# Performance work log

Measured on AMD Instinct MI355X. Metric: run time of the kernel, lower is better.

The kernel has to match this reference:

```python
import jax, jax.numpy as jnp
import numpy as np

D = 1024      # n_embd
H = 2048      # expert_hidden_dim
G = 4         # num_groups
EPG = 2       # experts_per_group
NH = 16       # num_heads
HD = D // NH  # head dim
L = 4         # num_layers
V = 32000     # vocab_size
NC = 32000    # num_classes
MAXS = 2048   # max_seq_len
B, S = 2, 1024
TEMP = 1.0    # router_temperature


def setup_inputs() -> dict:
    key = jax.random.key(0)
    ks = jax.random.split(key, 12)
    sc = 0.02
    def n(k, shape):
        return jax.random.normal(k, shape, jnp.float32) * sc
    return {
        "x": jax.random.randint(ks[0], (B, S), 0, V),
        "tok_emb": n(ks[1], (V, D)),
        "pos_emb": n(ks[2], (MAXS, D)),
        "in_proj_w": n(ks[3], (L, 3 * D, D)),
        "in_proj_b": jnp.zeros((L, 3 * D)),
        "out_w": n(ks[4], (L, D, D)),
        "out_b": jnp.zeros((L, D)),
        "ln1_w": jnp.ones((L, D)), "ln1_b": jnp.zeros((L, D)),
        "ln2_w": jnp.ones((L, D)), "ln2_b": jnp.zeros((L, D)),
        "gr_w": n(ks[5], (L, D, G)), "gr_b": jnp.zeros((L, G)),
        "er_w": n(ks[6], (L, G, D, EPG)), "er_b": jnp.zeros((L, G, EPG)),
        "w1": n(ks[7], (L, G, EPG, D, H)), "b1": jnp.zeros((L, G, EPG, H)),
        "w2": n(ks[8], (L, G, EPG, H, D)), "b2": jnp.zeros((L, G, EPG, D)),
        "lnf_w": jnp.ones((D,)), "lnf_b": jnp.zeros((D,)),
        "head_w": n(ks[9], (NC, D)), "head_b": jnp.zeros((NC,)),
    }


def _ln(x, w, b):
    m = x.mean(-1, keepdims=True)
    v = ((x - m) ** 2).mean(-1, keepdims=True)
    return (x - m) * jax.lax.rsqrt(v + 1e-5) * w + b


def _attn(x, wqkv, bqkv, wo, bo, mask):
    b, s, _ = x.shape
    qkv = x @ wqkv.T + bqkv
    q, k, v = jnp.split(qkv, 3, axis=-1)
    def heads(t):
        return t.reshape(b, s, NH, HD).transpose(0, 2, 1, 3)
    q, k, v = heads(q), heads(k), heads(v)
    sc = jnp.einsum('bhqd,bhkd->bhqk', q, k) / np.float32(np.sqrt(HD))
    sc = jnp.where(mask, sc, jnp.float32(-1e30))
    a = jax.nn.softmax(sc, axis=-1)
    o = jnp.einsum('bhqk,bhkd->bhqd', a, v).transpose(0, 2, 1, 3).reshape(b, s, D)
    return o @ wo.T + bo


def _moe(x, gw, gb, ew, eb, w1, b1, w2, b2):
    # x: [T, D] flattened tokens. 2-level routing: top-1 group, top-1 expert in group.
    gp = jax.nn.softmax((x @ gw + gb) / TEMP, axis=-1)                      # [T,G]
    gidx = jnp.argmax(gp, axis=-1)                                          # [T]
    ep = jax.nn.softmax((jnp.einsum('td,gde->tge', x, ew) + eb) / TEMP, -1)  # [T,G,EPG]
    ep_sel = jnp.take_along_axis(ep, gidx[:, None, None], axis=1)[:, 0]     # [T,EPG]
    eidx = jnp.argmax(ep_sel, axis=-1)                                      # [T]
    gate = (jnp.take_along_axis(gp, gidx[:, None], 1)[:, 0]
            * jnp.take_along_axis(ep_sel, eidx[:, None], 1)[:, 0])          # [T]
    hmid = jax.nn.relu(jnp.einsum('td,gedh->tgeh', x, w1) + b1)             # [T,G,EPG,H]
    out = jnp.einsum('tgeh,gehd->tged', hmid, w2) + b2                      # [T,G,EPG,D]
    comb = (jax.nn.one_hot(gidx, G, dtype=x.dtype)[:, :, None]
            * jax.nn.one_hot(eidx, EPG, dtype=x.dtype)[:, None, :]) * gate[:, None, None]
    return jnp.einsum('tge,tged->td', comb, out)


def reference(x, tok_emb, pos_emb, in_proj_w, in_proj_b, out_w, out_b,
              ln1_w, ln1_b, ln2_w, ln2_b, gr_w, gr_b, er_w, er_b,
              w1, b1, w2, b2, lnf_w, lnf_b, head_w, head_b):
    b, s = x.shape
    h = tok_emb[x] + pos_emb[jnp.arange(s)][None]
    mask = jnp.tril(jnp.ones((s, s), bool))
    for l in range(L):
        x1 = _ln(h, ln1_w[l], ln1_b[l])
        h = h + _attn(x1, in_proj_w[l], in_proj_b[l], out_w[l], out_b[l], mask)
        x2 = _ln(h, ln2_w[l], ln2_b[l]).reshape(b * s, D)
        h = h + _moe(x2, gr_w[l], gr_b[l], er_w[l], er_b[l],
                     w1[l], b1[l], w2[l], b2[l]).reshape(b, s, D)
    h = _ln(h, lnf_w, lnf_b).mean(axis=1)
    return h @ head_w.T + head_b
```

## Files before the change

kernel.cpp:

```cpp
#include <hip/hip_runtime.h>
#include <hip/hip_bf16.h>
#include <cstdint>
#include <cstddef>

#define D_   1024
#define H_   2048
#define G_   4
#define EPG_ 2
#define NE_  8
#define NH_  16
#define HD_  64
#define L_   4
#define V_   32000
#define NC_  32000
#define B_   2
#define S_   1024
#define T_   2048

typedef __attribute__((__ext_vector_type__(8))) __bf16 bf16x8;
typedef __attribute__((__ext_vector_type__(4))) __bf16 bf16x4;
typedef __attribute__((__ext_vector_type__(4))) float  f32x4;

__device__ __forceinline__ void gl_lds16(const void* g, void* l) {
  __builtin_amdgcn_global_load_lds(
      (const __attribute__((address_space(1))) void*)g,
      (__attribute__((address_space(3))) void*)l, 16, 0, 0);
}

__global__ __launch_bounds__(256) void embed_kernel(const int* __restrict__ x,
    const float* __restrict__ tok, const float* __restrict__ pos,
    float* __restrict__ h) {
  int t = blockIdx.x;
  int tid = threadIdx.x;
  int token = x[t];
  int s = t & (S_ - 1);
  float4 tv = *(const float4*)(tok + (size_t)token * D_ + tid * 4);
  float4 pv = *(const float4*)(pos + (size_t)s * D_ + tid * 4);
  float4 r;
  r.x = tv.x + pv.x; r.y = tv.y + pv.y; r.z = tv.z + pv.z; r.w = tv.w + pv.w;
  *(float4*)(h + (size_t)t * D_ + tid * 4) = r;
}

__device__ __forceinline__ float block_sum256(float v, float* sbuf) {
  #pragma unroll
  for (int o = 32; o >= 1; o >>= 1) v += __shfl_xor(v, o, 64);
  int tid = threadIdx.x;
  if ((tid & 63) == 0) sbuf[tid >> 6] = v;
  __syncthreads();
  float r = sbuf[0] + sbuf[1] + sbuf[2] + sbuf[3];
  __syncthreads();
  return r;
}

template<bool F32OUT, bool BFOUT>
__global__ __launch_bounds__(256) void ln_kernel(const float* __restrict__ X,
    const float* __restrict__ w, const float* __restrict__ b,
    float* __restrict__ Yf, __bf16* __restrict__ Yb) {
  __shared__ float sbuf[4];
  int t = blockIdx.x, tid = threadIdx.x;
  const float* xr = X + (size_t)t * D_;
  float4 v = *(const float4*)(xr + tid * 4);
  float sum = v.x + v.y + v.z + v.w;
  float m = block_sum256(sum, sbuf) * (1.0f / D_);
  float dx = v.x - m, dy = v.y - m, dz = v.z - m, dw = v.w - m;
  float vs = dx * dx + dy * dy + dz * dz + dw * dw;
  float var = block_sum256(vs, sbuf) * (1.0f / D_);
  float rs = rsqrtf(var + 1e-5f);
  float4 wv = *(const float4*)(w + tid * 4);
  float4 bv = *(const float4*)(b + tid * 4);
  float4 o;
  o.x = dx * rs * wv.x + bv.x;
  o.y = dy * rs * wv.y + bv.y;
  o.z = dz * rs * wv.z + bv.z;
  o.w = dw * rs * wv.w + bv.w;
  if (F32OUT) *(float4*)(Yf + (size_t)t * D_ + tid * 4) = o;
  if (BFOUT) {
    bf16x4 ob = {(__bf16)o.x, (__bf16)o.y, (__bf16)o.z, (__bf16)o.w};
    *(bf16x4*)(Yb + (size_t)t * D_ + tid * 4) = ob;
  }
}

template<int MODE, int NF, bool KN>
__global__ __launch_bounds__(256) void gemm_mfma(
    const __bf16* __restrict__ A, const float* __restrict__ W,
    const float* __restrict__ bias, float* __restrict__ Cf,
    __bf16* __restrict__ Cb, const int* __restrict__ tlist,
    const int* __restrict__ offs, const int* __restrict__ counts,
    const float* __restrict__ gate, int N, int K) {
  __shared__ __bf16 As[128 * 64];
  __shared__ __bf16 Bs[NF * 32 * 64];
  int e = blockIdx.z;
  int cnt = (MODE >= 2) ? counts[e] : T_;
  int row0 = blockIdx.y * 128;
  if (row0 >= cnt) return;
  int lbase = (MODE >= 2) ? offs[e] : 0;
  int col0 = blockIdx.x * (NF * 32);
  const float* Wp = W + (size_t)e * N * K;
  const float* bp = bias + (size_t)e * N;
  int tid = threadIdx.x;
  int w = tid >> 6, lane = tid & 63, lq = lane & 15, lg = lane >> 4;
  int wr = w >> 1, wc = w & 1;

  const __bf16* asrc[4];
  #pragma unroll
  for (int it = 0; it < 4; it++) {
    int v = it * 256 + tid;
    int r = v >> 3, u = v & 7;
    int gr = row0 + r;
    long rowidx;
    if (MODE >= 2) rowidx = tlist[lbase + ((gr < cnt) ? gr : cnt - 1)];
    else rowidx = gr;
    asrc[it] = A + (size_t)rowidx * K + (u ^ (r & 7)) * 8;
  }
  const float* bsrc[NF];
  int bdst[NF];
  #pragma unroll
  for (int it = 0; it < NF; it++) {
    if (!KN) {
      int v = it * 256 + tid;
      int n = v >> 3, u = v & 7;
      bsrc[it] = Wp + (size_t)(col0 + n) * K + u * 8;
      bdst[it] = n * 64 + (u ^ (n & 7)) * 8;
    } else {
      int v = it * 256 + tid;
      int n = v & (NF * 32 - 1), u = v / (NF * 32);
      bsrc[it] = Wp + (size_t)(u * 8) * N + col0 + n;
      bdst[it] = n * 64 + (u ^ (n & 7)) * 8;
    }
  }

  f32x4 acc[4][NF] = {};
  for (int k0 = 0; k0 < K; k0 += 64) {
    #pragma unroll
    for (int it = 0; it < 4; it++)
      gl_lds16(asrc[it] + k0, &As[(it * 256 + tid) * 8]);
    #pragma unroll
    for (int it = 0; it < NF; it++) {
      float f[8];
      if (!KN) {
        float4 f0 = *(const float4*)(bsrc[it] + k0);
        float4 f1 = *(const float4*)(bsrc[it] + k0 + 4);
        f[0] = f0.x; f[1] = f0.y; f[2] = f0.z; f[3] = f0.w;
        f[4] = f1.x; f[5] = f1.y; f[6] = f1.z; f[7] = f1.w;
      } else {
        #pragma unroll
        for (int j = 0; j < 8; j++)
          f[j] = bsrc[it][(size_t)(k0 + j) * N];
      }
      bf16x8 bb = {(__bf16)f[0], (__bf16)f[1], (__bf16)f[2], (__bf16)f[3],
                   (__bf16)f[4], (__bf16)f[5], (__bf16)f[6], (__bf16)f[7]};
      *(bf16x8*)&Bs[bdst[it]] = bb;
    }
    __syncthreads();
    #pragma unroll
    for (int kk = 0; kk < 2; kk++) {
      bf16x8 a[4], b[NF];
      int us = ((lg + kk * 4) ^ (lq & 7)) * 8;
      #pragma unroll
      for (int fi = 0; fi < 4; fi++)
        a[fi] = *(const bf16x8*)&As[(wr * 64 + fi * 16 + lq) * 64 + us];
      #pragma unroll
      for (int fj = 0; fj < NF; fj++)
        b[fj] = *(const bf16x8*)&Bs[(wc * (NF * 16) + fj * 16 + lq) * 64 + us];
      #pragma unroll
      for (int fi = 0; fi < 4; fi++)
        #pragma unroll
        for (int fj = 0; fj < NF; fj++)
          acc[fi][fj] = __builtin_amdgcn_mfma_f32_16x16x32_bf16(a[fi], b[fj], acc[fi][fj], 0, 0, 0);
    }
    __syncthreads();
  }

  #pragma unroll
  for (int fi = 0; fi < 4; fi++) {
    #pragma unroll
    for (int v = 0; v < 4; v++) {
      int r = row0 + wr * 64 + fi * 16 + lg * 4 + v;
      long orow;
      float gv = 1.f;
      if (MODE >= 2) {
        if (r >= cnt) continue;
        orow = tlist[lbase + r];
        if (MODE == 3) gv = gate[orow];
      } else {
        orow = r;
      }
      #pragma unroll
      for (int fj = 0; fj < NF; fj++) {
        int c = col0 + wc * (NF * 16) + fj * 16 + lq;
        float val = acc[fi][fj][v] + bp[c];
        if (MODE == 0)      Cb[orow * N + c] = (__bf16)val;
        else if (MODE == 1) Cf[orow * N + c] += val;
        else if (MODE == 2) Cb[orow * N + c] = (__bf16)fmaxf(val, 0.f);
        else                Cf[orow * N + c] += gv * val;
      }
    }
  }
}

#define SC_LOG2 0.18033688011112042f
__global__ __launch_bounds__(256) void attn_mfma_kernel(const __bf16* __restrict__ qkv,
                                                        __bf16* __restrict__ out) {
  __shared__ __bf16 Ks[64][72];
  __shared__ __bf16 Vt[64][72];
  __shared__ __bf16 Ps[64][72];
  int tid = threadIdx.x;
  int w = tid >> 6, lane = tid & 63, lq = lane & 15, lg = lane >> 4;
  int qt = blockIdx.x, b = blockIdx.y >> 4, hh = blockIdx.y & 15;
  const __bf16* qbase = qkv + (size_t)b * S_ * 3 * D_ + hh * HD_;

  bf16x8 qa[2];
  {
    const __bf16* qp = qbase + (size_t)(qt * 64 + w * 16 + lq) * 3 * D_ + lg * 8;
    qa[0] = *(const bf16x8*)qp;
    qa[1] = *(const bf16x8*)(qp + 32);
  }

  f32x4 o[4] = {};
  float m_[4] = {-1e30f, -1e30f, -1e30f, -1e30f};
  float l_[4] = {0.f, 0.f, 0.f, 0.f};

  for (int kt = 0; kt <= qt; kt++) {
    #pragma unroll
    for (int it = 0; it < 2; it++) {
      int idx = tid + it * 256;
      int row = idx >> 3, c8 = idx & 7;
      const __bf16* kp = qbase + (size_t)(kt * 64 + row) * 3 * D_ + D_ + c8 * 8;
      *(bf16x8*)&Ks[row][c8 * 8] = *(const bf16x8*)kp;
      bf16x8 vv = *(const bf16x8*)(kp + D_);
      #pragma unroll
      for (int j = 0; j < 8; j++) Vt[c8 * 8 + j][row] = vv[j];
    }
    __syncthreads();

    f32x4 s[4] = {};
    #pragma unroll
    for (int kk = 0; kk < 2; kk++)
      #pragma unroll
      for (int fc = 0; fc < 4; fc++) {
        bf16x8 kf = *(const bf16x8*)&Ks[fc * 16 + lq][lg * 8 + kk * 32];
        s[fc] = __builtin_amdgcn_mfma_f32_16x16x32_bf16(qa[kk], kf, s[fc], 0, 0, 0);
      }

    #pragma unroll
    for (int fc = 0; fc < 4; fc++)
      #pragma unroll
      for (int v = 0; v < 4; v++) {
        float sv = s[fc][v] * SC_LOG2;
        if (kt == qt && (fc * 16 + lq) > (w * 16 + lg * 4 + v)) sv = -1e30f;
        s[fc][v] = sv;
      }

    float corr[4];
    #pragma unroll
    for (int v = 0; v < 4; v++) {
      float rm = fmaxf(fmaxf(s[0][v], s[1][v]), fmaxf(s[2][v], s[3][v]));
      #pragma unroll
      for (int o2 = 8; o2 >= 1; o2 >>= 1) rm = fmaxf(rm, __shfl_xor(rm, o2, 64));
      float mnew = fmaxf(m_[v], rm);
      float cc = exp2f(m_[v] - mnew);
      float rs = 0.f;
      #pragma unroll
      for (int fc = 0; fc < 4; fc++) {
        float p = exp2f(s[fc][v] - mnew);
        s[fc][v] = p; rs += p;
      }
      l_[v] = l_[v] * cc + rs;
      m_[v] = mnew;
      corr[v] = cc;
    }
    #pragma unroll
    for (int dc = 0; dc < 4; dc++)
      #pragma unroll
      for (int v = 0; v < 4; v++) o[dc][v] *= corr[v];

    #pragma unroll
    for (int fc = 0; fc < 4; fc++)
      #pragma unroll
      for (int v = 0; v < 4; v++)
        Ps[w * 16 + lg * 4 + v][fc * 16 + lq] = (__bf16)s[fc][v];
    __syncthreads();

    #pragma unroll
    for (int kk = 0; kk < 2; kk++) {
      bf16x8 pa = *(const bf16x8*)&Ps[w * 16 + lq][lg * 8 + kk * 32];
      #pragma unroll
      for (int dc = 0; dc < 4; dc++) {
        bf16x8 vb = *(const bf16x8*)&Vt[dc * 16 + lq][lg * 8 + kk * 32];
        o[dc] = __builtin_amdgcn_mfma_f32_16x16x32_bf16(pa, vb, o[dc], 0, 0, 0);
      }
    }
    __syncthreads();
  }

  #pragma unroll
  for (int v = 0; v < 4; v++) {
    float ls = l_[v];
    #pragma unroll
    for (int o2 = 8; o2 >= 1; o2 >>= 1) ls += __shfl_xor(ls, o2, 64);
    float inv = 1.0f / ls;
    int row = qt * 64 + w * 16 + lg * 4 + v;
    __bf16* op = out + ((size_t)b * S_ + row) * D_ + hh * HD_;
    #pragma unroll
    for (int dc = 0; dc < 4; dc++)
      op[dc * 16 + lq] = (__bf16)(o[dc][v] * inv);
  }
}

__global__ __launch_bounds__(64) void route_kernel(const float* __restrict__ X,
    const float* __restrict__ gw, const float* __restrict__ gb,
    const float* __restrict__ ew, const float* __restrict__ eb,
    int* __restrict__ eidx, float* __restrict__ gate) {
  int t = blockIdx.x;
  int lane = threadIdx.x;
  const float* xr = X + (size_t)t * D_;
  float g0 = 0, g1 = 0, g2 = 0, g3 = 0;
  #pragma unroll
  for (int k = 0; k < 16; k++) {
    int d = lane + 64 * k;
    float xv = xr[d];
    float4 gv = *(const float4*)(gw + (size_t)d * G_);
    g0 += xv * gv.x; g1 += xv * gv.y; g2 += xv * gv.z; g3 += xv * gv.w;
  }
  #pragma unroll
  for (int o = 32; o >= 1; o >>= 1) {
    g0 += __shfl_xor(g0, o, 64); g1 += __shfl_xor(g1, o, 64);
    g2 += __shfl_xor(g2, o, 64); g3 += __shfl_xor(g3, o, 64);
  }
  g0 += gb[0]; g1 += gb[1]; g2 += gb[2]; g3 += gb[3];
  float mx = fmaxf(fmaxf(g0, g1), fmaxf(g2, g3));
  float p0 = __expf(g0 - mx), p1 = __expf(g1 - mx), p2 = __expf(g2 - mx), p3 = __expf(g3 - mx);
  float psum = p0 + p1 + p2 + p3;
  int gidx = 0; float best = g0;
  if (g1 > best) { best = g1; gidx = 1; }
  if (g2 > best) { best = g2; gidx = 2; }
  if (g3 > best) { best = g3; gidx = 3; }
  float gpsel = ((gidx == 0) ? p0 : (gidx == 1) ? p1 : (gidx == 2) ? p2 : p3) / psum;

  const float* ewg = ew + (size_t)gidx * D_ * EPG_;
  float e0 = 0, e1 = 0;
  #pragma unroll
  for (int k = 0; k < 16; k++) {
    int d = lane + 64 * k;
    float xv = xr[d];
    float2 ev = *(const float2*)(ewg + (size_t)d * EPG_);
    e0 += xv * ev.x; e1 += xv * ev.y;
  }
  #pragma unroll
  for (int o = 32; o >= 1; o >>= 1) {
    e0 += __shfl_xor(e0, o, 64); e1 += __shfl_xor(e1, o, 64);
  }
  e0 += eb[gidx * EPG_ + 0]; e1 += eb[gidx * EPG_ + 1];
  float em = fmaxf(e0, e1);
  float q0 = __expf(e0 - em), q1 = __expf(e1 - em);
  int ei = (e1 > e0) ? 1 : 0;
  float epsel = ((ei == 0) ? q0 : q1) / (q0 + q1);
  if (lane == 0) {
    eidx[t] = gidx * EPG_ + ei;
    gate[t] = gpsel * epsel;
  }
}

__global__ __launch_bounds__(256) void finalize_kernel(const int* __restrict__ eidx,
    int* __restrict__ counts, int* __restrict__ offs, int* __restrict__ tlist) {
  __shared__ int hist[256][NE_];
  __shared__ int eoff[NE_];
  int tid = threadIdx.x;
  int loc[NE_];
  #pragma unroll
  for (int e = 0; e < NE_; e++) loc[e] = 0;
  int te[8];
  #pragma unroll
  for (int i = 0; i < 8; i++) { te[i] = eidx[tid * 8 + i]; loc[te[i]]++; }
  #pragma unroll
  for (int e = 0; e < NE_; e++) hist[tid][e] = loc[e];
  __syncthreads();
  for (int off = 1; off < 256; off <<= 1) {
    int v[NE_];
    #pragma unroll
    for (int e = 0; e < NE_; e++) v[e] = (tid >= off) ? hist[tid - off][e] : 0;
    __syncthreads();
    #pragma unroll
    for (int e = 0; e < NE_; e++) hist[tid][e] += v[e];
    __syncthreads();
  }
  if (tid == 0) {
    int acc = 0;
    for (int e = 0; e < NE_; e++) {
      int c = hist[255][e];
      eoff[e] = acc; counts[e] = c; offs[e] = acc; acc += c;
    }
  }
  __syncthreads();
  int run[NE_];
  #pragma unroll
  for (int e = 0; e < NE_; e++) run[e] = eoff[e] + hist[tid][e] - loc[e];
  #pragma unroll
  for (int i = 0; i < 8; i++) {
    int e = te[i];
    tlist[run[e]++] = tid * 8 + i;
  }
}

__global__ __launch_bounds__(256) void mean_part_kernel(const float* __restrict__ X,
                                                        float* __restrict__ part) {
  int bd = blockIdx.x * 256 + threadIdx.x;
  int chunk = blockIdx.y;
  int b = bd >> 10, d = bd & 1023;
  float s = 0.f;
  #pragma unroll 4
  for (int i = 0; i < 64; i++) {
    int sidx = chunk * 64 + i;
    s += X[((size_t)b * S_ + sidx) * D_ + d];
  }
  part[chunk * T_ + bd] = s;
}

__global__ __launch_bounds__(256) void mean_final_kernel(const float* __restrict__ part,
                                                         float* __restrict__ hm) {
  int bd = blockIdx.x * 256 + threadIdx.x;
  float s = 0.f;
  #pragma unroll
  for (int c = 0; c < 16; c++) s += part[c * T_ + bd];
  hm[bd] = s * (1.0f / S_);
}

__global__ __launch_bounds__(256) void head_kernel(const float* __restrict__ hm,
    const float* __restrict__ hw, const float* __restrict__ hb,
    float* __restrict__ out) {
  int w = threadIdx.x >> 6;
  int lane = threadIdx.x & 63;
  int c = blockIdx.x * 4 + w;
  const float* row = hw + (size_t)c * D_;
  float acc0 = 0.f, acc1 = 0.f;
  #pragma unroll
  for (int k = 0; k < 4; k++) {
    int d = lane * 4 + k * 256;
    float4 wv = *(const float4*)(row + d);
    float4 h0 = *(const float4*)(hm + d);
    float4 h1 = *(const float4*)(hm + D_ + d);
    acc0 += wv.x * h0.x + wv.y * h0.y + wv.z * h0.z + wv.w * h0.w;
    acc1 += wv.x * h1.x + wv.y * h1.y + wv.z * h1.z + wv.w * h1.w;
  }
  #pragma unroll
  for (int o = 32; o >= 1; o >>= 1) {
    acc0 += __shfl_xor(acc0, o, 64);
    acc1 += __shfl_xor(acc1, o, 64);
  }
  if (lane == 0) {
    float bias = hb[c];
    out[c] = acc0 + bias;
    out[NC_ + c] = acc1 + bias;
  }
}

extern "C" void kernel_launch(void* const* d_in, const int* in_sizes, int n_in,
                              void* d_out, int out_size, void* d_ws, size_t ws_size,
                              hipStream_t stream) {
  const int*   x        = (const int*)d_in[0];
  const float* tok_emb  = (const float*)d_in[1];
  const float* pos_emb  = (const float*)d_in[2];
  const float* in_proj_w= (const float*)d_in[3];
  const float* in_proj_b= (const float*)d_in[4];
  const float* out_w    = (const float*)d_in[5];
  const float* out_b    = (const float*)d_in[6];
  const float* ln1_w    = (const float*)d_in[7];
  const float* ln1_b    = (const float*)d_in[8];
  const float* ln2_w    = (const float*)d_in[9];
  const float* ln2_b    = (const float*)d_in[10];
  const float* gr_w     = (const float*)d_in[11];
  const float* gr_b     = (const float*)d_in[12];
  const float* er_w     = (const float*)d_in[13];
  const float* er_b     = (const float*)d_in[14];
  const float* w1       = (const float*)d_in[15];
  const float* b1       = (const float*)d_in[16];
  const float* w2       = (const float*)d_in[17];
  const float* b2       = (const float*)d_in[18];
  const float* lnf_w    = (const float*)d_in[19];
  const float* lnf_b    = (const float*)d_in[20];
  const float* head_w   = (const float*)d_in[21];
  const float* head_b   = (const float*)d_in[22];

  char* wp = (char*)d_ws;
  auto carve = [&](size_t bytes) -> char* {
    char* p = wp;
    wp += (bytes + 255) & ~(size_t)255;
    return p;
  };
  float*  h      = (float*)carve((size_t)T_ * D_ * 4);
  float*  x1     = (float*)carve((size_t)T_ * D_ * 4);
  __bf16* x1b    = (__bf16*)carve((size_t)T_ * D_ * 2);
  __bf16* qkvb   = (__bf16*)carve((size_t)T_ * 3 * D_ * 2);
  __bf16* attnb  = (__bf16*)carve((size_t)T_ * D_ * 2);
  __bf16* hmidb  = (__bf16*)carve((size_t)T_ * H_ * 2);
  float*  part   = (float*)carve((size_t)16 * T_ * 4);
  float*  hm     = (float*)carve((size_t)B_ * D_ * 4);
  float*  gate   = (float*)carve((size_t)T_ * 4);
  int*    eidx   = (int*)carve((size_t)T_ * 4);
  int*    tlist  = (int*)carve((size_t)T_ * 4);
  int*    counts = (int*)carve(64);
  int*    offs   = (int*)carve(64);

  embed_kernel<<<T_, 256, 0, stream>>>(x, tok_emb, pos_emb, h);

  for (int l = 0; l < L_; l++) {
    ln_kernel<false, true><<<T_, 256, 0, stream>>>(h, ln1_w + l * D_, ln1_b + l * D_,
                                                   nullptr, x1b);
    gemm_mfma<0, 4, false><<<dim3(24, 16, 1), 256, 0, stream>>>(
        x1b, in_proj_w + (size_t)l * 3 * D_ * D_, in_proj_b + (size_t)l * 3 * D_,
        nullptr, qkvb, nullptr, nullptr, nullptr, nullptr, 3 * D_, D_);
    attn_mfma_kernel<<<dim3(S_ / 64, B_ * NH_), 256, 0, stream>>>(qkvb, attnb);
    gemm_mfma<1, 2, false><<<dim3(16, 16, 1), 256, 0, stream>>>(
        attnb, out_w + (size_t)l * D_ * D_, out_b + (size_t)l * D_, h, nullptr,
        nullptr, nullptr, nullptr, nullptr, D_, D_);

    ln_kernel<true, true><<<T_, 256, 0, stream>>>(h, ln2_w + l * D_, ln2_b + l * D_,
                                                  x1, x1b);
    route_kernel<<<T_, 64, 0, stream>>>(x1,
        gr_w + (size_t)l * D_ * G_, gr_b + (size_t)l * G_,
        er_w + (size_t)l * G_ * D_ * EPG_, er_b + (size_t)l * G_ * EPG_,
        eidx, gate);
    finalize_kernel<<<1, 256, 0, stream>>>(eidx, counts, offs, tlist);

    gemm_mfma<2, 4, true><<<dim3(H_ / 128, T_ / 128, NE_), 256, 0, stream>>>(
        x1b, w1 + (size_t)l * NE_ * D_ * H_, b1 + (size_t)l * NE_ * H_, nullptr, hmidb,
        tlist, offs, counts, nullptr, H_, D_);
    gemm_mfma<3, 2, true><<<dim3(D_ / 64, T_ / 128, NE_), 256, 0, stream>>>(
        hmidb, w2 + (size_t)l * NE_ * H_ * D_, b2 + (size_t)l * NE_ * D_, h, nullptr,
        tlist, offs, counts, gate, D_, H_);
  }

  ln_kernel<true, false><<<T_, 256, 0, stream>>>(h, lnf_w, lnf_b, x1, nullptr);
  mean_part_kernel<<<dim3(B_ * D_ / 256, 16), 256, 0, stream>>>(x1, part);
  mean_final_kernel<<<B_ * D_ / 256, 256, 0, stream>>>(part, hm);
  head_kernel<<<NC_ / 4, 256, 0, stream>>>(hm, head_w, head_b, (float*)d_out);
}
```

Measured before the change: 1.037 ms.

## Fuse LN2 with routing, compact MoE tile grid, prefetch GEMM weights, reverse attention order

LayerNorm2 and the two-level router are merged into one kernel that keeps the normalized row in registers, removing the fp32 x1 round trip and one launch. The finalize step now emits a compact list of (expert, row-tile) blocks, so the expert GEMMs launch at most 24 row tiles instead of an 8x16 grid that mostly exits early. The GEMM main loop double-buffers the fp32 weight loads in registers so the next tile's global reads overlap the current MFMA phase, and launch bounds request two blocks per CU. Attention blocks are issued in reverse query-tile order so the longest causal tiles start first. The register prefetch raises register pressure and could limit occupancy.

```diff
diff --git a/kernel.cpp b/kernel.cpp
--- a/kernel.cpp
+++ b/kernel.cpp
@@ -16,6 +16,7 @@
 #define B_   2
 #define S_   1024
 #define T_   2048
+#define MAXBLK_ 24
 
 typedef __attribute__((__ext_vector_type__(8))) __bf16 bf16x8;
 typedef __attribute__((__ext_vector_type__(4))) __bf16 bf16x4;
@@ -25,6 +26,12 @@
   __builtin_amdgcn_global_load_lds(
       (const __attribute__((address_space(1))) void*)g,
       (__attribute__((address_space(3))) void*)l, 16, 0, 0);
+}
+
+__device__ __forceinline__ float wave_sum(float v) {
+  #pragma unroll
+  for (int o = 32; o >= 1; o >>= 1) v += __shfl_xor(v, o, 64);
+  return v;
 }
 
 __global__ __launch_bounds__(256) void embed_kernel(const int* __restrict__ x,
@@ -42,8 +49,7 @@
 }
 
 __device__ __forceinline__ float block_sum256(float v, float* sbuf) {
-  #pragma unroll
-  for (int o = 32; o >= 1; o >>= 1) v += __shfl_xor(v, o, 64);
+  v = wave_sum(v);
   int tid = threadIdx.x;
   if ((tid & 63) == 0) sbuf[tid >> 6] = v;
   __syncthreads();
@@ -80,19 +86,147 @@
   }
 }
 
+__global__ __launch_bounds__(256) void ln_route_kernel(const float* __restrict__ X,
+    const float* __restrict__ lw, const float* __restrict__ lb,
+    const float* __restrict__ gw, const float* __restrict__ gb,
+    const float* __restrict__ ew, const float* __restrict__ eb,
+    __bf16* __restrict__ Yb, int* __restrict__ eidx, float* __restrict__ gate) {
+  int wv = threadIdx.x >> 6, lane = threadIdx.x & 63;
+  int t = blockIdx.x * 4 + wv;
+  const float* xr = X + (size_t)t * D_;
+  float4 xv[4];
+  #pragma unroll
+  for (int k = 0; k < 4; k++) xv[k] = *(const float4*)(xr + lane * 4 + k * 256);
+  float s = 0.f;
+  #pragma unroll
+  for (int k = 0; k < 4; k++) s += xv[k].x + xv[k].y + xv[k].z + xv[k].w;
+  float m = wave_sum(s) * (1.0f / D_);
+  float vs = 0.f;
+  #pragma unroll
+  for (int k = 0; k < 4; k++) {
+    float a = xv[k].x - m, b2 = xv[k].y - m, c = xv[k].z - m, d = xv[k].w - m;
+    vs += a * a + b2 * b2 + c * c + d * d;
+  }
+  float rs = rsqrtf(wave_sum(vs) * (1.0f / D_) + 1e-5f);
+  float y[4][4];
+  #pragma unroll
+  for (int k = 0; k < 4; k++) {
+    int d0 = lane * 4 + k * 256;
+    float4 wv4 = *(const float4*)(lw + d0);
+    float4 bv4 = *(const float4*)(lb + d0);
+    y[k][0] = (xv[k].x - m) * rs * wv4.x + bv4.x;
+    y[k][1] = (xv[k].y - m) * rs * wv4.y + bv4.y;
+    y[k][2] = (xv[k].z - m) * rs * wv4.z + bv4.z;
+    y[k][3] = (xv[k].w - m) * rs * wv4.w + bv4.w;
+    bf16x4 ob = {(__bf16)y[k][0], (__bf16)y[k][1], (__bf16)y[k][2], (__bf16)y[k][3]};
+    *(bf16x4*)(Yb + (size_t)t * D_ + d0) = ob;
+  }
+  float g0 = 0, g1 = 0, g2 = 0, g3 = 0;
+  #pragma unroll
+  for (int k = 0; k < 4; k++)
+    #pragma unroll
+    for (int j = 0; j < 4; j++) {
+      int d = lane * 4 + k * 256 + j;
+      float4 gv = *(const float4*)(gw + (size_t)d * G_);
+      float yv = y[k][j];
+      g0 += yv * gv.x; g1 += yv * gv.y; g2 += yv * gv.z; g3 += yv * gv.w;
+    }
+  g0 = wave_sum(g0) + gb[0];
+  g1 = wave_sum(g1) + gb[1];
+  g2 = wave_sum(g2) + gb[2];
+  g3 = wave_sum(g3) + gb[3];
+  float mx = fmaxf(fmaxf(g0, g1), fmaxf(g2, g3));
+  float p0 = __expf(g0 - mx), p1 = __expf(g1 - mx), p2 = __expf(g2 - mx), p3 = __expf(g3 - mx);
+  float psum = p0 + p1 + p2 + p3;
+  int gidx = 0; float best = g0;
+  if (g1 > best) { best = g1; gidx = 1; }
+  if (g2 > best) { best = g2; gidx = 2; }
+  if (g3 > best) { best = g3; gidx = 3; }
+  float gpsel = ((gidx == 0) ? p0 : (gidx == 1) ? p1 : (gidx == 2) ? p2 : p3) / psum;
+  const float* ewg = ew + (size_t)gidx * D_ * EPG_;
+  float e0 = 0, e1 = 0;
+  #pragma unroll
+  for (int k = 0; k < 4; k++)
+    #pragma unroll
+    for (int j = 0; j < 4; j++) {
+      int d = lane * 4 + k * 256 + j;
+      float2 ev = *(const float2*)(ewg + (size_t)d * EPG_);
+      e0 += y[k][j] * ev.x; e1 += y[k][j] * ev.y;
+    }
+  e0 = wave_sum(e0) + eb[gidx * EPG_ + 0];
+  e1 = wave_sum(e1) + eb[gidx * EPG_ + 1];
+  float em = fmaxf(e0, e1);
+  float q0 = __expf(e0 - em), q1 = __expf(e1 - em);
+  int ei = (e1 > e0) ? 1 : 0;
+  float epsel = ((ei == 0) ? q0 : q1) / (q0 + q1);
+  if (lane == 0) {
+    eidx[t] = gidx * EPG_ + ei;
+    gate[t] = gpsel * epsel;
+  }
+}
+
+__global__ __launch_bounds__(256) void finalize_kernel(const int* __restrict__ eidx,
+    int* __restrict__ counts, int* __restrict__ offs, int* __restrict__ tlist,
+    int* __restrict__ blk) {
+  __shared__ int hist[256][NE_];
+  __shared__ int eoff[NE_];
+  int tid = threadIdx.x;
+  int loc[NE_];
+  #pragma unroll
+  for (int e = 0; e < NE_; e++) loc[e] = 0;
+  int te[8];
+  #pragma unroll
+  for (int i = 0; i < 8; i++) { te[i] = eidx[tid * 8 + i]; loc[te[i]]++; }
+  #pragma unroll
+  for (int e = 0; e < NE_; e++) hist[tid][e] = loc[e];
+  __syncthreads();
+  for (int off = 1; off < 256; off <<= 1) {
+    int v[NE_];
+    #pragma unroll
+    for (int e = 0; e < NE_; e++) v[e] = (tid >= off) ? hist[tid - off][e] : 0;
+    __syncthreads();
+    #pragma unroll
+    for (int e = 0; e < NE_; e++) hist[tid][e] += v[e];
+    __syncthreads();
+  }
+  if (tid == 0) {
+    int acc = 0, nb = 0;
+    for (int e = 0; e < NE_; e++) {
+      int c = hist[255][e];
+      eoff[e] = acc; counts[e] = c; offs[e] = acc; acc += c;
+      for (int mt = 0; mt * 128 < c; mt++) blk[nb++] = e | (mt << 8);
+    }
+    for (; nb < MAXBLK_; nb++) blk[nb] = -1;
+  }
+  __syncthreads();
+  int run[NE_];
+  #pragma unroll
+  for (int e = 0; e < NE_; e++) run[e] = eoff[e] + hist[tid][e] - loc[e];
+  #pragma unroll
+  for (int i = 0; i < 8; i++) {
+    int e = te[i];
+    tlist[run[e]++] = tid * 8 + i;
+  }
+}
+
 template<int MODE, int NF, bool KN>
-__global__ __launch_bounds__(256) void gemm_mfma(
+__global__ __launch_bounds__(256, 2) void gemm_mfma(
     const __bf16* __restrict__ A, const float* __restrict__ W,
     const float* __restrict__ bias, float* __restrict__ Cf,
     __bf16* __restrict__ Cb, const int* __restrict__ tlist,
     const int* __restrict__ offs, const int* __restrict__ counts,
-    const float* __restrict__ gate, int N, int K) {
+    const float* __restrict__ gate, const int* __restrict__ blk,
+    int N, int K) {
   __shared__ __bf16 As[128 * 64];
   __shared__ __bf16 Bs[NF * 32 * 64];
-  int e = blockIdx.z;
-  int cnt = (MODE >= 2) ? counts[e] : T_;
-  int row0 = blockIdx.y * 128;
-  if (row0 >= cnt) return;
+  int e = 0, mt = blockIdx.y, cnt = T_;
+  if (MODE >= 2) {
+    int bv = blk[blockIdx.y];
+    if (bv < 0) return;
+    e = bv & 255; mt = bv >> 8;
+    cnt = counts[e];
+  }
+  int row0 = mt * 128;
   int lbase = (MODE >= 2) ? offs[e] : 0;
   int col0 = blockIdx.x * (NF * 32);
   const float* Wp = W + (size_t)e * N * K;
@@ -129,29 +263,42 @@
     }
   }
 
+  float br0[NF * 8], br1[NF * 8];
   f32x4 acc[4][NF] = {};
-  for (int k0 = 0; k0 < K; k0 += 64) {
-    #pragma unroll
-    for (int it = 0; it < 4; it++)
-      gl_lds16(asrc[it] + k0, &As[(it * 256 + tid) * 8]);
+
+  auto loadB = [&](float* br, int k0) {
     #pragma unroll
     for (int it = 0; it < NF; it++) {
-      float f[8];
       if (!KN) {
         float4 f0 = *(const float4*)(bsrc[it] + k0);
         float4 f1 = *(const float4*)(bsrc[it] + k0 + 4);
-        f[0] = f0.x; f[1] = f0.y; f[2] = f0.z; f[3] = f0.w;
-        f[4] = f1.x; f[5] = f1.y; f[6] = f1.z; f[7] = f1.w;
+        br[it * 8 + 0] = f0.x; br[it * 8 + 1] = f0.y;
+        br[it * 8 + 2] = f0.z; br[it * 8 + 3] = f0.w;
+        br[it * 8 + 4] = f1.x; br[it * 8 + 5] = f1.y;
+        br[it * 8 + 6] = f1.z; br[it * 8 + 7] = f1.w;
       } else {
         #pragma unroll
         for (int j = 0; j < 8; j++)
-          f[j] = bsrc[it][(size_t)(k0 + j) * N];
+          br[it * 8 + j] = bsrc[it][(size_t)(k0 + j) * N];
       }
-      bf16x8 bb = {(__bf16)f[0], (__bf16)f[1], (__bf16)f[2], (__bf16)f[3],
-                   (__bf16)f[4], (__bf16)f[5], (__bf16)f[6], (__bf16)f[7]};
+    }
+  };
+  auto writeB = [&](const float* br) {
+    #pragma unroll
+    for (int it = 0; it < NF; it++) {
+      bf16x8 bb = {(__bf16)br[it * 8 + 0], (__bf16)br[it * 8 + 1],
+                   (__bf16)br[it * 8 + 2], (__bf16)br[it * 8 + 3],
+                   (__bf16)br[it * 8 + 4], (__bf16)br[it * 8 + 5],
+                   (__bf16)br[it * 8 + 6], (__bf16)br[it * 8 + 7]};
       *(bf16x8*)&Bs[bdst[it]] = bb;
     }
-    __syncthreads();
+  };
+  auto stageA = [&](int k0) {
+    #pragma unroll
+    for (int it = 0; it < 4; it++)
+      gl_lds16(asrc[it] + k0, &As[(it * 256 + tid) * 8]);
+  };
+  auto mfmaPhase = [&]() {
     #pragma unroll
     for (int kk = 0; kk < 2; kk++) {
       bf16x8 a[4], b[NF];
@@ -168,6 +315,21 @@
         for (int fj = 0; fj < NF; fj++)
           acc[fi][fj] = __builtin_amdgcn_mfma_f32_16x16x32_bf16(a[fi], b[fj], acc[fi][fj], 0, 0, 0);
     }
+  };
+
+  loadB(br0, 0);
+  for (int k0 = 0; k0 < K; k0 += 128) {
+    stageA(k0);
+    writeB(br0);
+    loadB(br1, k0 + 64);
+    __syncthreads();
+    mfmaPhase();
+    __syncthreads();
+    stageA(k0 + 64);
+    writeB(br1);
+    if (k0 + 128 < K) loadB(br0, k0 + 128);
+    __syncthreads();
+    mfmaPhase();
     __syncthreads();
   }
 
@@ -206,7 +368,8 @@
   __shared__ __bf16 Ps[64][72];
   int tid = threadIdx.x;
   int w = tid >> 6, lane = tid & 63, lq = lane & 15, lg = lane >> 4;
-  int qt = blockIdx.x, b = blockIdx.y >> 4, hh = blockIdx.y & 15;
+  int qt = (S_ / 64 - 1) - blockIdx.x;
+  int b = blockIdx.y >> 4, hh = blockIdx.y & 15;
   const __bf16* qbase = qkv + (size_t)b * S_ * 3 * D_ + hh * HD_;
 
   bf16x8 qa[2];
@@ -304,101 +467,6 @@
     #pragma unroll
     for (int dc = 0; dc < 4; dc++)
       op[dc * 16 + lq] = (__bf16)(o[dc][v] * inv);
-  }
-}
-
-__global__ __launch_bounds__(64) void route_kernel(const float* __restrict__ X,
-    const float* __restrict__ gw, const float* __restrict__ gb,
-    const float* __restrict__ ew, const float* __restrict__ eb,
-    int* __restrict__ eidx, float* __restrict__ gate) {
-  int t = blockIdx.x;
-  int lane = threadIdx.x;
-  const float* xr = X + (size_t)t * D_;
-  float g0 = 0, g1 = 0, g2 = 0, g3 = 0;
-  #pragma unroll
-  for (int k = 0; k < 16; k++) {
-    int d = lane + 64 * k;
-    float xv = xr[d];
-    float4 gv = *(const float4*)(gw + (size_t)d * G_);
-    g0 += xv * gv.x; g1 += xv * gv.y; g2 += xv * gv.z; g3 += xv * gv.w;
-  }
-  #pragma unroll
-  for (int o = 32; o >= 1; o >>= 1) {
-    g0 += __shfl_xor(g0, o, 64); g1 += __shfl_xor(g1, o, 64);
-    g2 += __shfl_xor(g2, o, 64); g3 += __shfl_xor(g3, o, 64);
-  }
-  g0 += gb[0]; g1 += gb[1]; g2 += gb[2]; g3 += gb[3];
-  float mx = fmaxf(fmaxf(g0, g1), fmaxf(g2, g3));
-  float p0 = __expf(g0 - mx), p1 = __expf(g1 - mx), p2 = __expf(g2 - mx), p3 = __expf(g3 - mx);
-  float psum = p0 + p1 + p2 + p3;
-  int gidx = 0; float best = g0;
-  if (g1 > best) { best = g1; gidx = 1; }
-  if (g2 > best) { best = g2; gidx = 2; }
-  if (g3 > best) { best = g3; gidx = 3; }
-  float gpsel = ((gidx == 0) ? p0 : (gidx == 1) ? p1 : (gidx == 2) ? p2 : p3) / psum;
-
-  const float* ewg = ew + (size_t)gidx * D_ * EPG_;
-  float e0 = 0, e1 = 0;
-  #pragma unroll
-  for (int k = 0; k < 16; k++) {
-    int d = lane + 64 * k;
-    float xv = xr[d];
-    float2 ev = *(const float2*)(ewg + (size_t)d * EPG_);
-    e0 += xv * ev.x; e1 += xv * ev.y;
-  }
-  #pragma unroll
-  for (int o = 32; o >= 1; o >>= 1) {
-    e0 += __shfl_xor(e0, o, 64); e1 += __shfl_xor(e1, o, 64);
-  }
-  e0 += eb[gidx * EPG_ + 0]; e1 += eb[gidx * EPG_ + 1];
-  float em = fmaxf(e0, e1);
-  float q0 = __expf(e0 - em), q1 = __expf(e1 - em);
-  int ei = (e1 > e0) ? 1 : 0;
-  float epsel = ((ei == 0) ? q0 : q1) / (q0 + q1);
-  if (lane == 0) {
-    eidx[t] = gidx * EPG_ + ei;
-    gate[t] = gpsel * epsel;
-  }
-}
-
-__global__ __launch_bounds__(256) void finalize_kernel(const int* __restrict__ eidx,
-    int* __restrict__ counts, int* __restrict__ offs, int* __restrict__ tlist) {
-  __shared__ int hist[256][NE_];
-  __shared__ int eoff[NE_];
-  int tid = threadIdx.x;
-  int loc[NE_];
-  #pragma unroll
-  for (int e = 0; e < NE_; e++) loc[e] = 0;
-  int te[8];
-  #pragma unroll
-  for (int i = 0; i < 8; i++) { te[i] = eidx[tid * 8 + i]; loc[te[i]]++; }
-  #pragma unroll
-  for (int e = 0; e < NE_; e++) hist[tid][e] = loc[e];
-  __syncthreads();
-  for (int off = 1; off < 256; off <<= 1) {
-    int v[NE_];
-    #pragma unroll
-    for (int e = 0; e < NE_; e++) v[e] = (tid >= off) ? hist[tid - off][e] : 0;
-    __syncthreads();
-    #pragma unroll
-    for (int e = 0; e < NE_; e++) hist[tid][e] += v[e];
-    __syncthreads();
-  }
-  if (tid == 0) {
-    int acc = 0;
-    for (int e = 0; e < NE_; e++) {
-      int c = hist[255][e];
-      eoff[e] = acc; counts[e] = c; offs[e] = acc; acc += c;
-    }
-  }
-  __syncthreads();
-  int run[NE_];
-  #pragma unroll
-  for (int e = 0; e < NE_; e++) run[e] = eoff[e] + hist[tid][e] - loc[e];
-  #pragma unroll
-  for (int i = 0; i < 8; i++) {
-    int e = te[i];
-    tlist[run[e]++] = tid * 8 + i;
   }
 }
 
@@ -500,6 +568,7 @@
   int*    tlist  = (int*)carve((size_t)T_ * 4);
   int*    counts = (int*)carve(64);
   int*    offs   = (int*)carve(64);
+  int*    blk    = (int*)carve(MAXBLK_ * 4);
 
   embed_kernel<<<T_, 256, 0, stream>>>(x, tok_emb, pos_emb, h);
 
@@ -508,26 +577,25 @@
                                                    nullptr, x1b);
     gemm_mfma<0, 4, false><<<dim3(24, 16, 1), 256, 0, stream>>>(
         x1b, in_proj_w + (size_t)l * 3 * D_ * D_, in_proj_b + (size_t)l * 3 * D_,
-        nullptr, qkvb, nullptr, nullptr, nullptr, nullptr, 3 * D_, D_);
+        nullptr, qkvb, nullptr, nullptr, nullptr, nullptr, nullptr, 3 * D_, D_);
     attn_mfma_kernel<<<dim3(S_ / 64, B_ * NH_), 256, 0, stream>>>(qkvb, attnb);
     gemm_mfma<1, 2, false><<<dim3(16, 16, 1), 256, 0, stream>>>(
         attnb, out_w + (size_t)l * D_ * D_, out_b + (size_t)l * D_, h, nullptr,
-        nullptr, nullptr, nullptr, nullptr, D_, D_);
-
-    ln_kernel<true, true><<<T_, 256, 0, stream>>>(h, ln2_w + l * D_, ln2_b + l * D_,
-                                                  x1, x1b);
-    route_kernel<<<T_, 64, 0, stream>>>(x1,
+        nullptr, nullptr, nullptr, nullptr, nullptr, D_, D_);
+
+    ln_route_kernel<<<T_ / 4, 256, 0, stream>>>(h,
+        ln2_w + l * D_, ln2_b + l * D_,
         gr_w + (size_t)l * D_ * G_, gr_b + (size_t)l * G_,
         er_w + (size_t)l * G_ * D_ * EPG_, er_b + (size_t)l * G_ * EPG_,
-        eidx, gate);
-    finalize_kernel<<<1, 256, 0, stream>>>(eidx, counts, offs, tlist);
-
-    gemm_mfma<2, 4, true><<<dim3(H_ / 128, T_ / 128, NE_), 256, 0, stream>>>(
+        x1b, eidx, gate);
+    finalize_kernel<<<1, 256, 0, stream>>>(eidx, counts, offs, tlist, blk);
+
+    gemm_mfma<2, 4, true><<<dim3(H_ / 128, MAXBLK_, 1), 256, 0, stream>>>(
         x1b, w1 + (size_t)l * NE_ * D_ * H_, b1 + (size_t)l * NE_ * H_, nullptr, hmidb,
-        tlist, offs, counts, nullptr, H_, D_);
-    gemm_mfma<3, 2, true><<<dim3(D_ / 64, T_ / 128, NE_), 256, 0, stream>>>(
+        tlist, offs, counts, nullptr, blk, H_, D_);
+    gemm_mfma<3, 2, true><<<dim3(D_ / 64, MAXBLK_, 1), 256, 0, stream>>>(
         hmidb, w2 + (size_t)l * NE_ * H_ * D_, b2 + (size_t)l * NE_ * D_, h, nullptr,
-        tlist, offs, counts, gate, D_, H_);
+        tlist, offs, counts, gate, blk, D_, H_);
   }
 
   ln_kernel<true, false><<<T_, 256, 0, stream>>>(h, lnf_w, lnf_b, x1, nullptr);
```

Result: faster. 906.0 us (-12.6%).
